# Kernel tuning notes

Hardware: AMD Instinct MI355X
Metric: run time of the kernel (lower is better)

## Reference

```python
import jax, jax.numpy as jnp
import numpy as np

EPS = 1e-5  # BatchNorm eps (eval mode)
K_MAIN = 10
K_CORR = 8
LRELU = 0.2


def _knn_idx(x, k):
    # x: [B, c, n] -> [B, n, k] indices of k nearest neighbors (negative sq. distance top-k)
    inner = -2.0 * jnp.einsum('bcn,bcm->bnm', x, x)
    xx = jnp.sum(x * x, axis=1)                      # [B, n]
    pd = -xx[:, :, None] - inner - xx[:, None, :]    # [B, n, n]
    return jax.lax.top_k(pd, k)[1]


def _gather_neighbors(x, idx):
    # x: [B, c, n], idx: [B, n, k] -> [B, n, k, c]
    xt = jnp.transpose(x, (0, 2, 1))
    B = x.shape[0]
    return xt[jnp.arange(B)[:, None, None], idx]


def _graph_feature(x, k):
    # torch get_graph_feature: cat(neighbor - center, center) -> [B, 2c, n, k]
    idx = _knn_idx(x, k)
    neigh = _gather_neighbors(x, idx)                 # [B, n, k, c]
    xt = jnp.transpose(x, (0, 2, 1))                  # [B, n, c]
    center = jnp.broadcast_to(xt[:, :, None, :], neigh.shape)
    feat = jnp.concatenate([neigh - center, center], axis=-1)
    return jnp.transpose(feat, (0, 3, 1, 2))


def _branch(feat, w, g, b, m, v):
    # 1x1 Conv2d (no bias) + BatchNorm2d (eval) + LeakyReLU(0.2)
    y = jnp.einsum('oc,bcnk->bonk', w, feat)
    s = (g / jnp.sqrt(v + EPS))[None, :, None, None]
    y = (y - m[None, :, None, None]) * s + b[None, :, None, None]
    return jnp.where(y > 0, y, LRELU * y)


def _erase(x, masks, soft, w_e, b_e, g_e, be_e, m_e, v_e):
    # erase_feature: masked-softmax attention pooling + 1x1 conv_erase (conv+BN)
    soft = soft - (1.0 - masks) * 1e8
    sm = jax.nn.softmax(soft, axis=1)                 # [B, n]
    inp = x * masks[:, None, :]
    res = jnp.einsum('bcn,bn->bc', x, sm)             # [B, c]
    y = jnp.einsum('oc,bc->bo', w_e, res) + b_e
    y = (y - m_e) * (g_e / jnp.sqrt(v_e + EPS)) + be_e
    return inp + y[:, :, None]


def _corre_binar(x0_, x2, w_reduce):
    # x0_: [B, c] (detached query), x2: [B, c, n]
    B, c, n = x2.shape
    q = jnp.einsum('oc,bc->bo', w_reduce, x0_)        # conv_reduce (1x1, no bias)
    scale = 1.0 / jnp.sqrt(jnp.asarray(c, x2.dtype))
    f = jnp.einsum('bc,bcn->bn', q, x2) * scale       # [B, n]
    idx8 = _knn_idx(x2, K_CORR)                       # [B, n, 8]
    neigh = _gather_neighbors(x2, idx8)               # [B, n, 8, c]
    fk = jnp.einsum('bc,bnkc->bnk', q, neigh) * scale
    fk = f + jnp.sum(fk, axis=-1)                     # [B, n]
    index = jnp.argmax(fk, axis=1)                    # [B]
    ib = jnp.arange(B)
    masks = jnp.zeros((B, n), x2.dtype).at[ib, index].set(1.0)
    index_k = idx8[ib, index]                         # [B, 8] neighbors of argmax point
    masks = masks.at[ib[:, None], index_k].set(1.0)
    return 1.0 - masks, f


def _forward(x, w_reduce, w_erase, b_erase, g_erase, be_erase, m_erase, v_erase,
             w0, g0, b0, m0, v0, w1, g1, b1, m1, v1):
    b, t, c, n = x.shape
    B = b * t
    x1seq = jnp.concatenate([x[:, 1:], x[:, -1:]], axis=1).reshape(B, c, n)
    ones = jnp.ones((B, n), x.dtype)
    x0 = _erase(x.reshape(B, c, n), ones, ones,
                w_erase, b_erase, g_erase, be_erase, m_erase, v_erase)
    y0 = jnp.max(_branch(_graph_feature(x0, K_MAIN), w0, g0, b0, m0, v0), axis=-1)  # [B, O, n]
    x0_vec = jnp.max(y0, axis=-1)                                                    # [B, O]
    p0 = jnp.concatenate([jnp.max(y0, axis=-1), jnp.mean(y0, axis=-1)], axis=1)
    masks, soft = _corre_binar(jax.lax.stop_gradient(x0_vec), x1seq, w_reduce)
    x1e = _erase(x1seq, masks, soft,
                 w_erase, b_erase, g_erase, be_erase, m_erase, v_erase)
    y1 = jnp.max(_branch(_graph_feature(x1e, K_MAIN), w1, g1, b1, m1, v1), axis=-1)
    p1 = jnp.concatenate([jnp.max(y1, axis=-1), jnp.mean(y1, axis=-1)], axis=1)
    return p0 + p1                                                                   # [B, 2*O]


def setup_inputs() -> dict:
    key = jax.random.key(0)
    ks = jax.random.split(key, 20)
    b, t, c, n, out = 8, 12, 64, 512, 64
    sc = np.sqrt(2.0 / c).astype(np.float32)
    scb = np.sqrt(2.0 / out).astype(np.float32)
    f32 = jnp.float32
    inp = {
        'x': jax.random.normal(ks[0], (b, t, c, n), f32),
        'w_reduce': jax.random.normal(ks[1], (c, c), f32) * sc,
        'w_erase': jax.random.normal(ks[2], (c, c), f32) * sc,
        'b_erase': jax.random.normal(ks[3], (c,), f32) * 0.01,
        'g_erase': jax.random.uniform(ks[4], (c,), f32, 0.5, 1.5),
        'be_erase': jax.random.normal(ks[5], (c,), f32) * 0.1,
        'm_erase': jax.random.normal(ks[6], (c,), f32) * 0.1,
        'v_erase': jax.random.uniform(ks[7], (c,), f32, 0.5, 1.5),
        'w0': jax.random.normal(ks[8], (out, 2 * c), f32) * scb,
        'g0': jax.random.uniform(ks[9], (out,), f32, 0.5, 1.5),
        'b0': jax.random.normal(ks[10], (out,), f32) * 0.1,
        'm0': jax.random.normal(ks[11], (out,), f32) * 0.1,
        'v0': jax.random.uniform(ks[12], (out,), f32, 0.5, 1.5),
        'w1': jax.random.normal(ks[13], (out, 2 * c), f32) * scb,
        'g1': jax.random.uniform(ks[14], (out,), f32, 0.5, 1.5),
        'b1': jax.random.normal(ks[15], (out,), f32) * 0.1,
        'm1': jax.random.normal(ks[16], (out,), f32) * 0.1,
        'v1': jax.random.uniform(ks[17], (out,), f32, 0.5, 1.5),
    }
    return inp


def reference(x, w_reduce, w_erase, b_erase, g_erase, be_erase, m_erase, v_erase,
              w0, g0, b0, m0, v0, w1, g1, b1, m1, v1):
    return _forward(x, w_reduce, w_erase, b_erase, g_erase, be_erase, m_erase, v_erase,
                    w0, g0, b0, m0, v0, w1, g1, b1, m1, v1)
```

## Files before the change

### kernel.cpp

```cpp
#include <hip/hip_runtime.h>
#include <math.h>

#define EPS 1e-5f

typedef _Float16 half8 __attribute__((ext_vector_type(8)));
typedef float f32x4 __attribute__((ext_vector_type(4)));


__device__ __forceinline__ int src_row(int bq) {
    int b = bq / 12, t = bq - b * 12;
    int t2 = (t + 1 < 12) ? (t + 1) : 11;
    return b * 12 + t2;
}

__global__ __launch_bounds__(256) void prep_kernel(
    const float* __restrict__ X,
    _Float16* __restrict__ H, _Float16* __restrict__ L, float* __restrict__ xn,
    const float* __restrict__ w0, const float* __restrict__ w1,
    _Float16* __restrict__ wh0, _Float16* __restrict__ wl0,
    _Float16* __restrict__ wh1, _Float16* __restrict__ wl1,
    const float* __restrict__ w_e, const float* __restrict__ b_e,
    const float* __restrict__ g_e, const float* __restrict__ be_e,
    const float* __restrict__ m_e, const float* __restrict__ v_e,
    float* __restrict__ bias0)
{
    __shared__ float lds[64 * 65];
    __shared__ float xnp[4 * 64];
    __shared__ float part[256];
    __shared__ float res[64];
    __shared__ float sy[64];
    int raw = blockIdx.x;
    int tid = threadIdx.x;
    if (raw >= 768) {
        int bq = raw - 768;
        int c = tid >> 2, p = tid & 3;
        const float* xb = X + (size_t)bq * 32768 + c * 512 + p * 128;
        float acc = 0.f;
        for (int ii = 0; ii < 128; ii += 4) {
            float4 v = *(const float4*)(xb + ii);
            acc += v.x + v.y + v.z + v.w;
        }
        part[tid] = acc;
        __syncthreads();
        if (p == 0) res[c] = (part[tid] + part[tid+1] + part[tid+2] + part[tid+3]) * (1.f/512.f);
        __syncthreads();
        if (tid < 64) {
            float a = b_e[tid];
            for (int cc = 0; cc < 64; ++cc) a += w_e[tid*64+cc] * res[cc];
            float s = g_e[tid] / sqrtf(v_e[tid] + EPS);
            sy[tid] = (a - m_e[tid]) * s + be_e[tid];
        }
        __syncthreads();
        if (tid < 64) {
            float a = 0.f;
            for (int cc = 0; cc < 64; ++cc) a += w0[tid * 128 + 64 + cc] * sy[cc];
            bias0[bq * 64 + tid] = a;
        }
        return;
    }
    int bq = raw % 96;
    int ct = raw / 96;
    const float* Xb = X + (size_t)bq * 32768 + ct * 64;
    for (int p = 0; p < 16; ++p) {
        int t = p * 256 + tid;
        int c = t >> 6, col = t & 63;
        lds[c * 65 + col] = Xb[c * 512 + col];
    }
    __syncthreads();
    int col = tid & 63, g = tid >> 6;
    half8 hv[2], lv[2];
    float s = 0.f;
    #pragma unroll
    for (int k = 0; k < 16; ++k) {
        int c = g * 16 + k;
        float v = lds[c * 65 + col];
        _Float16 h = (_Float16)v;
        _Float16 lo = (_Float16)(v - (float)h);
        hv[k >> 3][k & 7] = h;
        lv[k >> 3][k & 7] = lo;
        s += v * v;
    }
    size_t obase = (size_t)bq * 32768 + ((size_t)(ct * 8 + 2 * g) * 64 + col) * 8;
    *(half8*)(H + obase) = hv[0];
    *(half8*)(H + obase + 512) = hv[1];
    *(half8*)(L + obase) = lv[0];
    *(half8*)(L + obase + 512) = lv[1];
    xnp[g * 64 + col] = s;
    __syncthreads();
    if (tid < 64)
        xn[bq * 512 + ct * 64 + tid] =
            xnp[tid] + xnp[64 + tid] + xnp[128 + tid] + xnp[192 + tid];
    if (raw < 2) {
        const float* W = raw ? w1 : w0;
        _Float16* WH = raw ? wh1 : wh0;
        _Float16* WL = raw ? wl1 : wl0;
        for (int t = tid; t < 8192; t += 256) {
            int o = t >> 6, c = t & 63;
            float v = (o < 64) ? W[o * 128 + c]
                               : (W[(o - 64) * 128 + 64 + c] - W[(o - 64) * 128 + c]);
            _Float16 h = (_Float16)v;
            WH[t] = h;
            WL[t] = (_Float16)(v - (float)h);
        }
    }
}

__global__ __launch_bounds__(256, 4) void knn_kernel(
    const _Float16* __restrict__ H, const _Float16* __restrict__ L,
    const float* __restrict__ xn,
    unsigned short* __restrict__ idx_out, unsigned short* __restrict__ key_out)
{
    __shared__ float4 jbuf[2048];
    __shared__ float sxn[512];
    int raw = blockIdx.x;
    int bq = raw % 96;
    int itile = raw / 96;
    int tid = threadIdx.x, w = tid >> 6, l = tid & 63;
    int lane16 = l & 15, quad = l >> 4;
    const size_t base = (size_t)bq * 32768;
    const _Float16* Hb = H + base;
    const _Float16* Lb = L + base;

    int irow = itile * 64 + w * 16 + lane16;
    size_t bo = ((size_t)(itile * 8 + quad) * 64 + (w * 16 + lane16)) * 8;
    half8 Bh0 = *(const half8*)(Hb + bo);
    half8 Bh1 = *(const half8*)(Hb + bo + 2048);
    half8 Bl0 = *(const half8*)(Lb + bo);
    half8 Bl1 = *(const half8*)(Lb + bo + 2048);

    unsigned kv[20];
    #pragma unroll
    for (int qq = 0; qq < 20; ++qq) kv[qq] = 0u;

    auto casu = [](unsigned& a, unsigned& b) {
        unsigned mn = __builtin_elementwise_min(a, b);
        unsigned mx = __builtin_elementwise_max(a, b);
        a = mn; b = mx;
    };

    const float* xnb = xn + bq * 512;
    float4* jbH = jbuf;
    float4* jbL = jbuf + 1024;
    {
        const float4* gh = (const float4*)(Hb);
        const float4* gl = (const float4*)(Lb);
        jbH[tid] = gh[tid]; jbH[256 + tid] = gh[256 + tid];
        jbL[tid] = gl[tid]; jbL[256 + tid] = gl[256 + tid];
        sxn[tid] = xnb[tid]; sxn[256 + tid] = xnb[256 + tid];
    }
    __syncthreads();
    for (int jt = 0; jt < 8; ++jt) {
        int cur = jt & 1;
        float4 pa0, pa1, pb0, pb1;
        if (jt < 7) {
            const float4* gh = (const float4*)(Hb + (jt + 1) * 4096);
            const float4* gl = (const float4*)(Lb + (jt + 1) * 4096);
            pa0 = gh[tid]; pa1 = gh[256 + tid];
            pb0 = gl[tid]; pb1 = gl[256 + tid];
        }
        const _Float16* jH = (const _Float16*)(jbH + cur * 512);
        const _Float16* jL = (const _Float16*)(jbL + cur * 512);
        unsigned scb = (unsigned)((7 - jt) << 4);
        unsigned d[16];
        #pragma unroll
        for (int g = 0; g < 4; ++g) {
            int u = quad * 64 + g * 16 + lane16;
            half8 Ah0 = *(const half8*)(jH + (size_t)u * 8);
            half8 Ah1 = *(const half8*)(jH + (size_t)u * 8 + 2048);
            half8 Al0 = *(const half8*)(jL + (size_t)u * 8);
            half8 Al1 = *(const half8*)(jL + (size_t)u * 8 + 2048);
            f32x4 acc = {0.f, 0.f, 0.f, 0.f};
            acc = __builtin_amdgcn_mfma_f32_16x16x32_f16(Ah0, Bh0, acc, 0, 0, 0);
            acc = __builtin_amdgcn_mfma_f32_16x16x32_f16(Ah1, Bh1, acc, 0, 0, 0);
            acc = __builtin_amdgcn_mfma_f32_16x16x32_f16(Al0, Bh0, acc, 0, 0, 0);
            acc = __builtin_amdgcn_mfma_f32_16x16x32_f16(Al1, Bh1, acc, 0, 0, 0);
            acc = __builtin_amdgcn_mfma_f32_16x16x32_f16(Ah0, Bl0, acc, 0, 0, 0);
            acc = __builtin_amdgcn_mfma_f32_16x16x32_f16(Ah1, Bl1, acc, 0, 0, 0);
            int jb = jt * 64 + g * 16 + quad * 4;
            float4 xn4 = *(const float4*)&sxn[jb];
            #pragma unroll
            for (int r = 0; r < 4; ++r) {
                float xnr = (r == 0 ? xn4.x : r == 1 ? xn4.y : r == 2 ? xn4.z : xn4.w);
                float sc = fmaf(2.f, acc[r], -xnr);
                int bi = __float_as_int(sc);
                unsigned u2 = (unsigned)(bi ^ ((bi >> 31) | 0x80000000));
                int slot = g * 4 + r;
                d[slot] = (u2 & 0xFFFFFF80u) | (scb | (unsigned)(15 - slot));
            }
        }
        #pragma unroll
        for (int p = 1; p < 16; p <<= 1) {
            #pragma unroll
            for (int k = p; k >= 1; k >>= 1) {
                #pragma unroll
                for (int j = k & (p - 1); j + k < 16; j += 2 * k) {
                    #pragma unroll
                    for (int i = 0; i < k; ++i) {
                        if ((i + j + k < 16) &&
                            ((i + j) / (2 * p) == (i + j + k) / (2 * p)))
                            casu(d[i + j], d[i + j + k]);
                    }
                }
            }
        }
        #pragma unroll
        for (int i = 0; i < 16; ++i)
            kv[i] = __builtin_elementwise_max(kv[i], d[15 - i]);
        casu(kv[0],kv[16]); casu(kv[1],kv[17]); casu(kv[2],kv[18]); casu(kv[3],kv[19]);
        casu(kv[0],kv[8]);  casu(kv[1],kv[9]);  casu(kv[2],kv[10]); casu(kv[3],kv[11]);
        casu(kv[4],kv[12]); casu(kv[5],kv[13]); casu(kv[6],kv[14]); casu(kv[7],kv[15]);
        casu(kv[0],kv[4]);  casu(kv[1],kv[5]);  casu(kv[2],kv[6]);  casu(kv[3],kv[7]);
        casu(kv[8],kv[12]); casu(kv[9],kv[13]); casu(kv[10],kv[14]); casu(kv[11],kv[15]);
        casu(kv[0],kv[2]);  casu(kv[1],kv[3]);  casu(kv[4],kv[6]);  casu(kv[5],kv[7]);
        casu(kv[8],kv[10]); casu(kv[9],kv[11]); casu(kv[12],kv[14]); casu(kv[13],kv[15]);
        casu(kv[16],kv[18]); casu(kv[17],kv[19]);
        casu(kv[0],kv[1]);  casu(kv[2],kv[3]);  casu(kv[4],kv[5]);  casu(kv[6],kv[7]);
        casu(kv[8],kv[9]);  casu(kv[10],kv[11]); casu(kv[12],kv[13]); casu(kv[14],kv[15]);
        casu(kv[16],kv[17]); casu(kv[18],kv[19]);

        if (jt < 7) {
            jbH[(1 - cur) * 512 + tid] = pa0; jbH[(1 - cur) * 512 + 256 + tid] = pa1;
            jbL[(1 - cur) * 512 + tid] = pb0; jbL[(1 - cur) * 512 + 256 + tid] = pb1;
        }
        __syncthreads();
    }
    unsigned* MVb = (unsigned*)jbuf;
    #pragma unroll
    for (int qq = 0; qq < 20; ++qq)
        MVb[w * 1344 + (lane16 * 4 + quad) * 21 + qq] = kv[qq];
    __syncthreads();
    if (quad == 0) {
        const unsigned* MV = (const unsigned*)jbuf + w * 1344 + lane16 * 84;
        int p0 = 19, p1 = 19, p2 = 19, p3 = 19;
        unsigned v0 = MV[19], v1 = MV[21 + 19], v2 = MV[42 + 19], v3 = MV[63 + 19];
        unsigned short* op = idx_out + ((size_t)bq * 512 + irow) * 20;
        unsigned short* kp = key_out + ((size_t)bq * 512 + irow) * 20;
        for (int t = 0; t < 20; ++t) {
            int bc = 0; unsigned bv = v0;
            if (v1 > bv) { bv = v1; bc = 1; }
            if (v2 > bv) { bv = v2; bc = 2; }
            if (v3 > bv) { bv = v3; bc = 3; }
            int bits = (int)(bv & 127u), jtv = 7 - (bits >> 4), cod = 15 - (bits & 15);
            int j = jtv * 64 + ((cod >> 2) << 4) + bc * 4 + (cod & 3);
            op[t] = (unsigned short)j;
            kp[t] = (unsigned short)(bv >> 16);
            if (bc == 0)      { --p0; v0 = MV[p0 < 0 ? 0 : p0]; }
            else if (bc == 1) { --p1; v1 = MV[21 + (p1 < 0 ? 0 : p1)]; }
            else if (bc == 2) { --p2; v2 = MV[42 + (p2 < 0 ? 0 : p2)]; }
            else              { --p3; v3 = MV[63 + (p3 < 0 ? 0 : p3)]; }
        }
    }
}

__global__ __launch_bounds__(1024) void derive_kernel(
    const float* __restrict__ x, const float* __restrict__ x0vec,
    const float* __restrict__ w_reduce,
    const unsigned short* __restrict__ idxA, const unsigned short* __restrict__ keyA,
    const float* __restrict__ xn,
    const float* __restrict__ w_e, const float* __restrict__ b_e,
    const float* __restrict__ g_e, const float* __restrict__ be_e,
    const float* __restrict__ m_e, const float* __restrict__ v_e,
    const float* __restrict__ w1,
    unsigned short* __restrict__ idxB, float* __restrict__ masks_out,
    float* __restrict__ bias1_out)
{
    __shared__ unsigned short sja[512 * 20];
    __shared__ unsigned short ska[512 * 20];
    __shared__ float ss[512];
    __shared__ float sw8[512];
    __shared__ float smask[512];
    __shared__ float xnl[512];
    __shared__ float pl[1024];
    __shared__ float sxv[64], sq[64], sres[64], syy[64];
    __shared__ float redv[8];
    __shared__ int   redi[8];
    __shared__ float redf[8];
    __shared__ float redf2[8];
    __shared__ int mlist[12];
    __shared__ int nmin[12];
    __shared__ int s_mcnt, s_need;

    int bq = blockIdx.x;
    int row = src_row(bq);
    int tid = threadIdx.x;
    int w = tid >> 6, l = tid & 63;
    const float* Xb = x + (size_t)row * 32768;

    {
        const unsigned* gja = (const unsigned*)(idxA + (size_t)row * 10240);
        const unsigned* gka = (const unsigned*)(keyA + (size_t)row * 10240);
        unsigned* dja = (unsigned*)sja;
        unsigned* dka = (unsigned*)ska;
        #pragma unroll
        for (int t = 0; t < 5; ++t) dja[t * 1024 + tid] = gja[t * 1024 + tid];
        #pragma unroll
        for (int t = 0; t < 5; ++t) dka[t * 1024 + tid] = gka[t * 1024 + tid];
    }
    if (tid < 512) { xnl[tid] = xn[row * 512 + tid]; smask[tid] = 1.0f; }
    if (tid < 64) sxv[tid] = x0vec[bq * 64 + tid];
    __syncthreads();
    {
        int o = tid >> 4, c0 = (tid & 15) * 4;
        const float* wr = w_reduce + o * 64 + c0;
        pl[tid] = wr[0]*sxv[c0] + wr[1]*sxv[c0+1] + wr[2]*sxv[c0+2] + wr[3]*sxv[c0+3];
    }
    __syncthreads();
    if (tid < 64) {
        float a = 0.f;
        #pragma unroll
        for (int s = 0; s < 16; ++s) a += pl[tid * 16 + s];
        sq[tid] = a;
    }
    __syncthreads();
    {
        int i = tid >> 1, h = tid & 1;
        float a = 0.f;
        #pragma unroll
        for (int k = 0; k < 32; ++k) {
            int c = h * 32 + k;
            a += sq[c] * Xb[c * 512 + i];
        }
        a += __shfl_xor(a, 1);
        if (h == 0) ss[i] = a * 0.125f;
    }
    __syncthreads();
    if (tid < 512) {
        float a = ss[tid];
        const unsigned short* ip = &sja[tid * 20];
        #pragma unroll
        for (int q = 0; q < 8; ++q) a += ss[ip[q]];
        sw8[tid] = a;
    }
    __syncthreads();
    {
        float bv = -3.4e38f; int bi = 0x7fffffff;
        if (tid < 512) { bv = sw8[tid]; bi = tid; }
        #pragma unroll
        for (int off = 32; off >= 1; off >>= 1) {
            float ov = __shfl_down(bv, off);
            int oi = __shfl_down(bi, off);
            if (ov > bv || (ov == bv && oi < bi)) { bv = ov; bi = oi; }
        }
        if (l == 0 && w < 8) { redv[w] = bv; redi[w] = bi; }
    }
    __syncthreads();
    if (tid == 0) {
        float Bv = redv[0]; int Bi = redi[0];
        for (int ww = 1; ww < 8; ++ww)
            if (redv[ww] > Bv || (redv[ww] == Bv && redi[ww] < Bi)) { Bv = redv[ww]; Bi = redi[ww]; }
        smask[Bi] = 0.f;
        const unsigned short* ip = &sja[Bi * 20];
        int c[9];
        c[0] = Bi;
        for (int q = 0; q < 8; ++q) { int j = ip[q]; smask[j] = 0.f; c[q + 1] = j; }
        for (int i2 = 1; i2 < 9; ++i2) {
            int v = c[i2]; int j2 = i2 - 1;
            while (j2 >= 0 && c[j2] > v) { c[j2 + 1] = c[j2]; --j2; }
            c[j2 + 1] = v;
        }
        int mc = 0, prev = -1;
        for (int i2 = 0; i2 < 9; ++i2)
            if (c[i2] != prev) { mlist[mc++] = c[i2]; prev = c[i2]; }
        s_mcnt = mc;
        s_need = 10 - mc;
    }
    __syncthreads();
    int mcreg = s_mcnt, need = s_need;
    float sval = -3.4e38f;
    if (tid < 512) {
        masks_out[bq * 512 + tid] = smask[tid];
        sval = ss[tid] - (1.f - smask[tid]) * 1e8f;
    }
    {
        float m = sval;
        #pragma unroll
        for (int off = 32; off >= 1; off >>= 1) m = fmaxf(m, __shfl_down(m, off));
        if (l == 0 && w < 8) redf[w] = m;
    }
    __syncthreads();
    float mx = fmaxf(fmaxf(fmaxf(redf[0], redf[1]), fmaxf(redf[2], redf[3])),
                     fmaxf(fmaxf(redf[4], redf[5]), fmaxf(redf[6], redf[7])));
// ... 34 lines not shown
    }
    __syncthreads();
    {
        int o = tid >> 4, c0 = (tid & 15) * 4;
        const float* wr = w_e + o * 64 + c0;
        pl[tid] = wr[0]*sres[c0] + wr[1]*sres[c0+1] + wr[2]*sres[c0+2] + wr[3]*sres[c0+3];
    }
    __syncthreads();
    if (tid < 64) {
        float a = b_e[tid];
        #pragma unroll
        for (int s = 0; s < 16; ++s) a += pl[tid * 16 + s];
        float sc2 = g_e[tid] / sqrtf(v_e[tid] + EPS);
        syy[tid] = (a - m_e[tid]) * sc2 + be_e[tid];
    }
    __syncthreads();
    {
        int o = tid >> 4, c0 = (tid & 15) * 4;
        const float* wr = w1 + o * 128 + 64 + c0;
        pl[tid] = wr[0]*syy[c0] + wr[1]*syy[c0+1] + wr[2]*syy[c0+2] + wr[3]*syy[c0+3];
    }
    __syncthreads();
    if (tid < 64) {
        float a = 0.f;
        #pragma unroll
        for (int s = 0; s < 16; ++s) a += pl[tid * 16 + s];
        bias1_out[bq * 64 + tid] = a;
    }
    if (w == 0) {
        float v[8]; int id[8];
        #pragma unroll
        for (int k = 0; k < 8; ++k) {
            int j = l * 8 + k;
            v[k] = (smask[j] != 0.f) ? xnl[j] : 3.4e38f;
            id[k] = j;
        }
        for (int r = 0; r < need; ++r) {
            float bv = v[0]; int bi = id[0];
            #pragma unroll
            for (int k = 1; k < 8; ++k)
                if (v[k] < bv || (v[k] == bv && id[k] < bi)) { bv = v[k]; bi = id[k]; }
            #pragma unroll
            for (int off = 32; off >= 1; off >>= 1) {
                float ov = __shfl_xor(bv, off);
                int oi = __shfl_xor(bi, off);
                if (ov < bv || (ov == bv && oi < bi)) { bv = ov; bi = oi; }
            }
            if (l == 0) nmin[r] = bi;
            #pragma unroll
            for (int k = 0; k < 8; ++k)
                if (id[k] == bi) v[k] = 3.4e38f;
        }
    }
    __syncthreads();
    if (tid < 512) {
        int i = tid;
        unsigned short tmp[10];
        if (smask[i] == 0.f) {
            int t2 = 0;
            for (int k2 = 0; k2 < mcreg; ++k2) tmp[t2++] = (unsigned short)mlist[k2];
            for (int r = 0; t2 < 10; ++r) tmp[t2++] = (unsigned short)nmin[r];
        } else {
            const unsigned short* ja = &sja[i * 20];
            const unsigned short* ka = &ska[i * 20];
            int pa = 0, pb = 0;
            for (int t2 = 0; t2 < 10; ++t2) {
                while (smask[ja[pa]] == 0.f) ++pa;
                unsigned kva = ka[pa];
                int jva = ja[pa];
                bool takeA = (pb >= mcreg) || (kva > 0x8000u) ||
                             (kva == 0x8000u && jva < mlist[pb]);
                if (takeA) { tmp[t2] = (unsigned short)jva; ++pa; }
                else       { tmp[t2] = (unsigned short)mlist[pb]; ++pb; }
            }
        }
        unsigned* op = (unsigned*)(idxB + (size_t)bq * 5120 + (size_t)i * 10);
        #pragma unroll
        for (int k2 = 0; k2 < 5; ++k2)
            op[k2] = (unsigned)tmp[2 * k2] | ((unsigned)tmp[2 * k2 + 1] << 16);
    }
}

template<int ACC>
__global__ void __attribute__((amdgpu_flat_work_group_size(256, 256), amdgpu_waves_per_eu(2, 4)))
fused_branch_kernel(
    const _Float16* __restrict__ H, const _Float16* __restrict__ L,
    const _Float16* __restrict__ WH, const _Float16* __restrict__ WL,
    const unsigned short* __restrict__ idx, int istride,
    const float* __restrict__ masks, int remap,
    const float* __restrict__ bias,
    const float* __restrict__ g, const float* __restrict__ bb,
    const float* __restrict__ mm, const float* __restrict__ vv,
    float* __restrict__ out_p, float* __restrict__ vec_out)
{
    __shared__ float ldsA[8 * 512];
    __shared__ float ldsB[8 * 512];
    __shared__ unsigned short ldsIdx[512 * 10];
    __shared__ float smask[512];
    int bq = blockIdx.x, ob = blockIdx.y * 8;
    int row = remap ? src_row(bq) : bq;
    bool use_mask = (masks != nullptr);
    int tid = threadIdx.x, w = tid >> 6, l = tid & 63;
    int lane16 = l & 15, quad = l >> 4;
    const size_t base = (size_t)row * 32768;
    unsigned idreg[10];
    if (istride == 10) {
        const unsigned* gp = (const unsigned*)idx + (size_t)bq * 2560;
        #pragma unroll
        for (int k = 0; k < 10; ++k) idreg[k] = gp[tid + k * 256];
    } else {
        const unsigned* gp = (const unsigned*)idx + (size_t)bq * 5120;
        #pragma unroll
        for (int k = 0; k < 10; ++k) {
            int d = tid + k * 256;
            int i = d / 5, r = d - i * 5;
            idreg[k] = gp[i * 10 + r];
        }
    }
    if (use_mask) {
        smask[tid] = masks[bq * 512 + tid];
        smask[tid + 256] = masks[bq * 512 + tid + 256];
        __syncthreads();
    }
    {
        int wrow = (lane16 < 8) ? (ob + lane16) : (64 + ob + (lane16 - 8));
        size_t woff = (size_t)wrow * 64 + quad * 8;
        half8 Ah0 = *(const half8*)(WH + woff);
        half8 Ah1 = *(const half8*)(WH + woff + 32);
        half8 Al0 = *(const half8*)(WL + woff);
        half8 Al1 = *(const half8*)(WL + woff + 32);
        float* dst = (quad < 2) ? ldsA : ldsB;
        int pb = (quad & 1) * 2;
        for (int k = 0; k < 8; ++k) {
            int it = w * 8 + k;
            size_t off = base + (((size_t)(it >> 2) * 8 + quad) * 64 + (it & 3) * 16 + lane16) * 8;
            half8 Xh0 = *(const half8*)(H + off);
            half8 Xh1 = *(const half8*)(H + off + 2048);
            half8 Xl0 = *(const half8*)(L + off);
            half8 Xl1 = *(const half8*)(L + off + 2048);
            if (use_mask) {
                float m = smask[it * 16 + lane16];
                if (m == 0.f) {
                    half8 z = {};
                    Xh0 = z; Xh1 = z; Xl0 = z; Xl1 = z;
                }
            }
            f32x4 acc = {0.f, 0.f, 0.f, 0.f};
            acc = __builtin_amdgcn_mfma_f32_16x16x32_f16(Ah0, Xh0, acc, 0, 0, 0);
            acc = __builtin_amdgcn_mfma_f32_16x16x32_f16(Ah1, Xh1, acc, 0, 0, 0);
            acc = __builtin_amdgcn_mfma_f32_16x16x32_f16(Ah0, Xl0, acc, 0, 0, 0);
            acc = __builtin_amdgcn_mfma_f32_16x16x32_f16(Ah1, Xl1, acc, 0, 0, 0);
            acc = __builtin_amdgcn_mfma_f32_16x16x32_f16(Al0, Xh0, acc, 0, 0, 0);
            acc = __builtin_amdgcn_mfma_f32_16x16x32_f16(Al1, Xh1, acc, 0, 0, 0);
            int j = it * 16 + lane16;
            #pragma unroll
            for (int r = 0; r < 4; ++r)
                dst[((pb + (r >> 1)) * 512 + j) * 2 + (r & 1)] = acc[r];
        }
    }
    {
        unsigned* dp = (unsigned*)ldsIdx;
        #pragma unroll
        for (int k = 0; k < 10; ++k) dp[tid + k * 256] = idreg[k];
    }
    __syncthreads();
    float ssr[2], str[2];
    #pragma unroll
    for (int oo = 0; oo < 2; ++oo) {
        int o = ob + w * 2 + oo;
        float sc = g[o] / sqrtf(vv[o] + EPS);
        ssr[oo] = sc;
        str[oo] = bb[o] - mm[o] * sc + bias[bq * 64 + o] * sc;
    }
    float omax[2], osum[2];
    #pragma unroll
    for (int oo = 0; oo < 2; ++oo) { omax[oo] = -3.4e38f; osum[oo] = 0.f; }
    const float2* A2 = ((const float2*)ldsA) + w * 512;
    const float2* B2 = ((const float2*)ldsB) + w * 512;
    for (int s = 0; s < 8; ++s) {
        int i = l + 64 * s;
        const unsigned* ip32 = (const unsigned*)ldsIdx + i * 5;
        unsigned pr0 = ip32[0], pr1 = ip32[1], pr2 = ip32[2], pr3 = ip32[3], pr4 = ip32[4];
        int idr[10];
        idr[0] = pr0 & 0xffff; idr[1] = pr0 >> 16;
        idr[2] = pr1 & 0xffff; idr[3] = pr1 >> 16;
        idr[4] = pr2 & 0xffff; idr[5] = pr2 >> 16;
        idr[6] = pr3 & 0xffff; idr[7] = pr3 >> 16;
        idr[8] = pr4 & 0xffff; idr[9] = pr4 >> 16;
        float2 v0 = A2[idr[0]];
        float mx0 = v0.x, mx1 = v0.y;
        #pragma unroll
        for (int q = 1; q < 10; ++q) {
            float2 vq = A2[idr[q]];
            mx0 = fmaxf(mx0, vq.x);
            mx1 = fmaxf(mx1, vq.y);
        }
        float2 bv = B2[i];
        float val0 = (mx0 + bv.x) * ssr[0] + str[0];
        float val1 = (mx1 + bv.y) * ssr[1] + str[1];
        float y0 = val0 > 0.f ? val0 : 0.2f * val0;
        float y1 = val1 > 0.f ? val1 : 0.2f * val1;
        omax[0] = fmaxf(omax[0], y0); osum[0] += y0;
        omax[1] = fmaxf(omax[1], y1); osum[1] += y1;
    }
    #pragma unroll
    for (int oo = 0; oo < 2; ++oo) {
        float M = omax[oo], S = osum[oo];
        #pragma unroll
        for (int off = 32; off >= 1; off >>= 1) {
            M = fmaxf(M, __shfl_down(M, off));
            S += __shfl_down(S, off);
        }
        if (l == 0) {
            int o = ob + w * 2 + oo;
            float* po = out_p + bq * 128;
            if (ACC) {
                po[o] += M;
                po[64 + o] += S * (1.f / 512.f);
            } else {
                po[o] = M;
                po[64 + o] = S * (1.f / 512.f);
                vec_out[bq * 64 + o] = M;
            }
        }
    }
}

extern "C" void kernel_launch(void* const* d_in, const int* in_sizes, int n_in,
                              void* d_out, int out_size, void* d_ws, size_t ws_size,
                              hipStream_t stream)
{
    const float* x        = (const float*)d_in[0];
    const float* w_reduce = (const float*)d_in[1];
    const float* w_erase  = (const float*)d_in[2];
    const float* b_erase  = (const float*)d_in[3];
    const float* g_erase  = (const float*)d_in[4];
    const float* be_erase = (const float*)d_in[5];
    const float* m_erase  = (const float*)d_in[6];
    const float* v_erase  = (const float*)d_in[7];
    const float* w0 = (const float*)d_in[8];
    const float* g0 = (const float*)d_in[9];
    const float* b0 = (const float*)d_in[10];
    const float* m0 = (const float*)d_in[11];
    const float* v0 = (const float*)d_in[12];
    const float* w1 = (const float*)d_in[13];
    const float* g1 = (const float*)d_in[14];
    const float* b1 = (const float*)d_in[15];
    const float* m1 = (const float*)d_in[16];
    const float* v1 = (const float*)d_in[17];
    float* out = (float*)d_out;
    char* ws = (char*)d_ws;

    _Float16* h0 = (_Float16*)(ws);
    _Float16* l0 = (_Float16*)(ws + 6291456);
    unsigned short* idxA = (unsigned short*)(ws + 12582912);
    unsigned short* keyA = (unsigned short*)(ws + 14548992);
    unsigned short* idxB = (unsigned short*)(ws + 16515072);
    float* xn0   = (float*)(ws + 17498112);
    float* bias0 = (float*)(ws + 17694720);
    float* bias1 = (float*)(ws + 17719296);
    float* x0vec = (float*)(ws + 17743872);
    float* masks = (float*)(ws + 17768448);
    _Float16* wh0 = (_Float16*)(ws + 17965056);
    _Float16* wl0 = (_Float16*)(ws + 17981440);
    _Float16* wh1 = (_Float16*)(ws + 17997824);
    _Float16* wl1 = (_Float16*)(ws + 18014208);

    (void)in_sizes; (void)n_in; (void)out_size; (void)ws_size;

    prep_kernel<<<864, 256, 0, stream>>>(x, h0, l0, xn0, w0, w1, wh0, wl0, wh1, wl1,
                                         w_erase, b_erase, g_erase, be_erase, m_erase, v_erase, bias0);
    knn_kernel<<<768, 256, 0, stream>>>(h0, l0, xn0, idxA, keyA);
    fused_branch_kernel<0><<<dim3(96, 8), 256, 0, stream>>>(h0, l0, wh0, wl0, idxA, 20,
                                                            nullptr, 0, bias0,
                                                            g0, b0, m0, v0, out, x0vec);
    derive_kernel<<<96, 1024, 0, stream>>>(x, x0vec, w_reduce, idxA, keyA, xn0,
                                           w_erase, b_erase, g_erase, be_erase, m_erase, v_erase,
                                           w1, idxB, masks, bias1);
    fused_branch_kernel<1><<<dim3(96, 8), 256, 0, stream>>>(h0, l0, wh1, wl1, idxB, 10,
                                                            masks, 1, bias1,
                                                            g1, b1, m1, v1, out, nullptr);
}
```

Measured before the change: 182.3 us.

## Precompute both branch conv projections inside kNN kernel and stream them to gather kernels

The per-point 1x1-conv projections for both edge-conv branches are now computed once per point inside the kNN kernel, reusing its already-loaded fp16 hi/lo registers, and written to four fp32 workspace buffers. The branch kernels no longer recompute the MFMA projections. They load the precomputed tiles from global memory, multiplying by the mask in the masked case. This removes duplicated MFMA work, since each branch kernel previously recomputed the projections for every output block. The cost is about 50 MB of extra workspace traffic, and the kNN kernel's occupancy hint drops from 4 to 3 blocks per EU.

Result: slower. 202.5 us (+11.1%).

```diff
diff --git a/kernel.cpp b/kernel.cpp
--- a/kernel.cpp
+++ b/kernel.cpp
@@ -105,10 +105,14 @@
     }
 }
 
-__global__ __launch_bounds__(256, 4) void knn_kernel(
+__global__ __launch_bounds__(256, 3) void knn_kernel(
     const _Float16* __restrict__ H, const _Float16* __restrict__ L,
     const float* __restrict__ xn,
-    unsigned short* __restrict__ idx_out, unsigned short* __restrict__ key_out)
+    unsigned short* __restrict__ idx_out, unsigned short* __restrict__ key_out,
+    const _Float16* __restrict__ wh0, const _Float16* __restrict__ wl0,
+    const _Float16* __restrict__ wh1, const _Float16* __restrict__ wl1,
+    float* __restrict__ c0A, float* __restrict__ c0B,
+    float* __restrict__ c1A, float* __restrict__ c1B)
 {
     __shared__ float4 jbuf[2048];
     __shared__ float sxn[512];
@@ -128,10 +132,6 @@
     half8 Bl0 = *(const half8*)(Lb + bo);
     half8 Bl1 = *(const half8*)(Lb + bo + 2048);
 
-    unsigned kv[20];
-    #pragma unroll
-    for (int qq = 0; qq < 20; ++qq) kv[qq] = 0u;
-
     auto casu = [](unsigned& a, unsigned& b) {
         unsigned mn = __builtin_elementwise_min(a, b);
         unsigned mx = __builtin_elementwise_max(a, b);
@@ -148,6 +148,41 @@
         jbL[tid] = gl[tid]; jbL[256 + tid] = gl[256 + tid];
         sxn[tid] = xnb[tid]; sxn[256 + tid] = xnb[256 + tid];
     }
+    {
+        int pb = (quad & 1) * 2;
+        #pragma unroll
+        for (int cv = 0; cv < 2; ++cv) {
+            const _Float16* WH = cv ? wh1 : wh0;
+            const _Float16* WL = cv ? wl1 : wl0;
+            float* dAp = (cv ? c1A : c0A) + (size_t)bq * 32768;
+            float* dBp = (cv ? c1B : c0B) + (size_t)bq * 32768;
+            float* dst = (quad < 2) ? dAp : dBp;
+            #pragma unroll
+            for (int ob8 = 0; ob8 < 8; ++ob8) {
+                int ob = ob8 * 8;
+                int wrow = (lane16 < 8) ? (ob + lane16) : (64 + ob + (lane16 - 8));
+                size_t woff = (size_t)wrow * 64 + quad * 8;
+                half8 Ah0 = *(const half8*)(WH + woff);
+                half8 Ah1 = *(const half8*)(WH + woff + 32);
+                half8 Al0 = *(const half8*)(WL + woff);
+                half8 Al1 = *(const half8*)(WL + woff + 32);
+                f32x4 acc = {0.f, 0.f, 0.f, 0.f};
+                acc = __builtin_amdgcn_mfma_f32_16x16x32_f16(Ah0, Bh0, acc, 0, 0, 0);
+                acc = __builtin_amdgcn_mfma_f32_16x16x32_f16(Ah1, Bh1, acc, 0, 0, 0);
+                acc = __builtin_amdgcn_mfma_f32_16x16x32_f16(Ah0, Bl0, acc, 0, 0, 0);
+                acc = __builtin_amdgcn_mfma_f32_16x16x32_f16(Ah1, Bl1, acc, 0, 0, 0);
+                acc = __builtin_amdgcn_mfma_f32_16x16x32_f16(Al0, Bh0, acc, 0, 0, 0);
+                acc = __builtin_amdgcn_mfma_f32_16x16x32_f16(Al1, Bh1, acc, 0, 0, 0);
+                float2 v01 = {acc[0], acc[1]};
+                float2 v23 = {acc[2], acc[3]};
+                *(float2*)(dst + ((size_t)((ob8 * 4 + pb) * 512 + irow) * 2)) = v01;
+                *(float2*)(dst + ((size_t)((ob8 * 4 + pb + 1) * 512 + irow) * 2)) = v23;
+            }
+        }
+    }
+    unsigned kv[20];
+    #pragma unroll
+    for (int qq = 0; qq < 20; ++qq) kv[qq] = 0u;
     __syncthreads();
     for (int jt = 0; jt < 8; ++jt) {
         int cur = jt & 1;
@@ -497,10 +532,8 @@
 }
 
 template<int ACC>
-__global__ void __attribute__((amdgpu_flat_work_group_size(256, 256), amdgpu_waves_per_eu(2, 4)))
-fused_branch_kernel(
-    const _Float16* __restrict__ H, const _Float16* __restrict__ L,
-    const _Float16* __restrict__ WH, const _Float16* __restrict__ WL,
+__global__ __launch_bounds__(256) void gather_branch_kernel(
+    const float* __restrict__ cA, const float* __restrict__ cB,
     const unsigned short* __restrict__ idx, int istride,
     const float* __restrict__ masks, int remap,
     const float* __restrict__ bias,
@@ -512,12 +545,10 @@
     __shared__ float ldsB[8 * 512];
     __shared__ unsigned short ldsIdx[512 * 10];
     __shared__ float smask[512];
-    int bq = blockIdx.x, ob = blockIdx.y * 8;
+    int bq = blockIdx.x, ob8 = blockIdx.y;
     int row = remap ? src_row(bq) : bq;
     bool use_mask = (masks != nullptr);
     int tid = threadIdx.x, w = tid >> 6, l = tid & 63;
-    int lane16 = l & 15, quad = l >> 4;
-    const size_t base = (size_t)row * 32768;
     unsigned idreg[10];
     if (istride == 10) {
         const unsigned* gp = (const unsigned*)idx + (size_t)bq * 2560;
@@ -532,45 +563,28 @@
             idreg[k] = gp[i * 10 + r];
         }
     }
+    const float* gA = cA + (size_t)row * 32768 + (size_t)ob8 * 4096;
+    const float* gB = cB + (size_t)row * 32768 + (size_t)ob8 * 4096;
     if (use_mask) {
         smask[tid] = masks[bq * 512 + tid];
         smask[tid + 256] = masks[bq * 512 + tid + 256];
         __syncthreads();
-    }
-    {
-        int wrow = (lane16 < 8) ? (ob + lane16) : (64 + ob + (lane16 - 8));
-        size_t woff = (size_t)wrow * 64 + quad * 8;
-        half8 Ah0 = *(const half8*)(WH + woff);
-        half8 Ah1 = *(const half8*)(WH + woff + 32);
-        half8 Al0 = *(const half8*)(WL + woff);
-        half8 Al1 = *(const half8*)(WL + woff + 32);
-        float* dst = (quad < 2) ? ldsA : ldsB;
-        int pb = (quad & 1) * 2;
-        for (int k = 0; k < 8; ++k) {
-            int it = w * 8 + k;
-            size_t off = base + (((size_t)(it >> 2) * 8 + quad) * 64 + (it & 3) * 16 + lane16) * 8;
-            half8 Xh0 = *(const half8*)(H + off);
-            half8 Xh1 = *(const half8*)(H + off + 2048);
-            half8 Xl0 = *(const half8*)(L + off);
-            half8 Xl1 = *(const half8*)(L + off + 2048);
-            if (use_mask) {
-                float m = smask[it * 16 + lane16];
-                if (m == 0.f) {
-                    half8 z = {};
-                    Xh0 = z; Xh1 = z; Xl0 = z; Xl1 = z;
-                }
-            }
-            f32x4 acc = {0.f, 0.f, 0.f, 0.f};
-            acc = __builtin_amdgcn_mfma_f32_16x16x32_f16(Ah0, Xh0, acc, 0, 0, 0);
-            acc = __builtin_amdgcn_mfma_f32_16x16x32_f16(Ah1, Xh1, acc, 0, 0, 0);
-            acc = __builtin_amdgcn_mfma_f32_16x16x32_f16(Ah0, Xl0, acc, 0, 0, 0);
-            acc = __builtin_amdgcn_mfma_f32_16x16x32_f16(Ah1, Xl1, acc, 0, 0, 0);
-            acc = __builtin_amdgcn_mfma_f32_16x16x32_f16(Al0, Xh0, acc, 0, 0, 0);
-            acc = __builtin_amdgcn_mfma_f32_16x16x32_f16(Al1, Xh1, acc, 0, 0, 0);
-            int j = it * 16 + lane16;
-            #pragma unroll
-            for (int r = 0; r < 4; ++r)
-                dst[((pb + (r >> 1)) * 512 + j) * 2 + (r & 1)] = acc[r];
+        #pragma unroll
+        for (int k = 0; k < 16; ++k) {
+            int t = tid + k * 256;
+            float m = smask[(t >> 1) & 511];
+            ldsA[t] = gA[t] * m;
+            ldsB[t] = gB[t] * m;
+        }
+    } else {
+        float4* dA4 = (float4*)ldsA;
+        float4* dB4 = (float4*)ldsB;
+        const float4* gA4 = (const float4*)gA;
+        const float4* gB4 = (const float4*)gB;
+        #pragma unroll
+        for (int k = 0; k < 4; ++k) {
+            dA4[tid + k * 256] = gA4[tid + k * 256];
+            dB4[tid + k * 256] = gB4[tid + k * 256];
         }
     }
     {
@@ -579,6 +593,7 @@
         for (int k = 0; k < 10; ++k) dp[tid + k * 256] = idreg[k];
     }
     __syncthreads();
+    int ob = ob8 * 8;
     float ssr[2], str[2];
     #pragma unroll
     for (int oo = 0; oo < 2; ++oo) {
@@ -680,19 +695,24 @@
     _Float16* wl0 = (_Float16*)(ws + 17981440);
     _Float16* wh1 = (_Float16*)(ws + 17997824);
     _Float16* wl1 = (_Float16*)(ws + 18014208);
+    float* c0A = (float*)(ws + 18030592);
+    float* c0B = (float*)(ws + 30613504);
+    float* c1A = (float*)(ws + 43196416);
+    float* c1B = (float*)(ws + 55779328);
 
     (void)in_sizes; (void)n_in; (void)out_size; (void)ws_size;
 
     prep_kernel<<<864, 256, 0, stream>>>(x, h0, l0, xn0, w0, w1, wh0, wl0, wh1, wl1,
                                          w_erase, b_erase, g_erase, be_erase, m_erase, v_erase, bias0);
-    knn_kernel<<<768, 256, 0, stream>>>(h0, l0, xn0, idxA, keyA);
-    fused_branch_kernel<0><<<dim3(96, 8), 256, 0, stream>>>(h0, l0, wh0, wl0, idxA, 20,
-                                                            nullptr, 0, bias0,
-                                                            g0, b0, m0, v0, out, x0vec);
+    knn_kernel<<<768, 256, 0, stream>>>(h0, l0, xn0, idxA, keyA,
+                                        wh0, wl0, wh1, wl1, c0A, c0B, c1A, c1B);
+    gather_branch_kernel<0><<<dim3(96, 8), 256, 0, stream>>>(c0A, c0B, idxA, 20,
+                                                             nullptr, 0, bias0,
+                                                             g0, b0, m0, v0, out, x0vec);
     derive_kernel<<<96, 1024, 0, stream>>>(x, x0vec, w_reduce, idxA, keyA, xn0,
                                            w_erase, b_erase, g_erase, be_erase, m_erase, v_erase,
                                            w1, idxB, masks, bias1);
-    fused_branch_kernel<1><<<dim3(96, 8), 256, 0, stream>>>(h0, l0, wh1, wl1, idxB, 10,
-                                                            masks, 1, bias1,
-                                                            g1, b1, m1, v1, out, nullptr);
+    gather_branch_kernel<1><<<dim3(96, 8), 256, 0, stream>>>(c1A, c1B, idxB, 10,
+                                                             masks, 1, bias1,
+                                                             g1, b1, m1, v1, out, nullptr);
 }
```

## Split KNN candidate range across two blocks and merge partial top-k downstream

Applied to the files above, without the earlier changes.

The KNN kernel now splits each row's 512 candidates into two halves handled by separate blocks, doubling the grid, halving LDS, and raising occupancy to 5 blocks per CU. The four per-quad sorted lists are merged with register shuffles and bitonic cleanup instead of an LDS-based serial merge, and each half writes 20 packed keys with the index embedded. Consumers (the fused branch kernel and derive kernel) merge the two partial top-20 lists themselves. This removes the serial scalar merge and LDS staging, but adds merge work and more global traffic in the consumers.

Result: slower. 189.1 us (+3.7%).

```diff
diff --git a/kernel.cpp b/kernel.cpp
--- a/kernel.cpp
+++ b/kernel.cpp
@@ -11,6 +11,25 @@
     int b = bq / 12, t = bq - b * 12;
     int t2 = (t + 1 < 12) ? (t + 1) : 11;
     return b * 12 + t2;
+}
+
+__device__ __forceinline__ void cleanup20(unsigned (&kv)[20]) {
+    auto casu = [](unsigned& a, unsigned& b) {
+        unsigned mn = __builtin_elementwise_min(a, b);
+        unsigned mx = __builtin_elementwise_max(a, b);
+        a = mn; b = mx;
+    };
+    casu(kv[0],kv[16]); casu(kv[1],kv[17]); casu(kv[2],kv[18]); casu(kv[3],kv[19]);
+    casu(kv[0],kv[8]);  casu(kv[1],kv[9]);  casu(kv[2],kv[10]); casu(kv[3],kv[11]);
+    casu(kv[4],kv[12]); casu(kv[5],kv[13]); casu(kv[6],kv[14]); casu(kv[7],kv[15]);
+    casu(kv[0],kv[4]);  casu(kv[1],kv[5]);  casu(kv[2],kv[6]);  casu(kv[3],kv[7]);
+    casu(kv[8],kv[12]); casu(kv[9],kv[13]); casu(kv[10],kv[14]); casu(kv[11],kv[15]);
+    casu(kv[0],kv[2]);  casu(kv[1],kv[3]);  casu(kv[4],kv[6]);  casu(kv[5],kv[7]);
+    casu(kv[8],kv[10]); casu(kv[9],kv[11]); casu(kv[12],kv[14]); casu(kv[13],kv[15]);
+    casu(kv[16],kv[18]); casu(kv[17],kv[19]);
+    casu(kv[0],kv[1]);  casu(kv[2],kv[3]);  casu(kv[4],kv[5]);  casu(kv[6],kv[7]);
+    casu(kv[8],kv[9]);  casu(kv[10],kv[11]); casu(kv[12],kv[13]); casu(kv[14],kv[15]);
+    casu(kv[16],kv[17]); casu(kv[18],kv[19]);
 }
 
 __global__ __launch_bounds__(256) void prep_kernel(
@@ -105,16 +124,18 @@
     }
 }
 
-__global__ __launch_bounds__(256, 4) void knn_kernel(
+__global__ __launch_bounds__(256, 5) void knn_kernel(
     const _Float16* __restrict__ H, const _Float16* __restrict__ L,
     const float* __restrict__ xn,
-    unsigned short* __restrict__ idx_out, unsigned short* __restrict__ key_out)
+    unsigned* __restrict__ key_out)
 {
-    __shared__ float4 jbuf[2048];
-    __shared__ float sxn[512];
+    __shared__ float4 jbuf[1024];
+    __shared__ float sxn[256];
     int raw = blockIdx.x;
-    int bq = raw % 96;
-    int itile = raw / 96;
+    int bq = raw >> 4;
+    int sub = raw & 15;
+    int itile = sub >> 1;
+    int half = sub & 1;
     int tid = threadIdx.x, w = tid >> 6, l = tid & 63;
     int lane16 = l & 15, quad = l >> 4;
     const size_t base = (size_t)bq * 32768;
@@ -128,39 +149,36 @@
     half8 Bl0 = *(const half8*)(Lb + bo);
     half8 Bl1 = *(const half8*)(Lb + bo + 2048);
 
-    unsigned kv[20];
-    #pragma unroll
-    for (int qq = 0; qq < 20; ++qq) kv[qq] = 0u;
-
     auto casu = [](unsigned& a, unsigned& b) {
         unsigned mn = __builtin_elementwise_min(a, b);
         unsigned mx = __builtin_elementwise_max(a, b);
         a = mn; b = mx;
     };
 
-    const float* xnb = xn + bq * 512;
-    float4* jbH = jbuf;
-    float4* jbL = jbuf + 1024;
-    {
-        const float4* gh = (const float4*)(Hb);
-        const float4* gl = (const float4*)(Lb);
-        jbH[tid] = gh[tid]; jbH[256 + tid] = gh[256 + tid];
-        jbL[tid] = gl[tid]; jbL[256 + tid] = gl[256 + tid];
-        sxn[tid] = xnb[tid]; sxn[256 + tid] = xnb[256 + tid];
-    }
-    __syncthreads();
-    for (int jt = 0; jt < 8; ++jt) {
-        int cur = jt & 1;
+    unsigned kv[20];
+    #pragma unroll
+    for (int qq = 0; qq < 20; ++qq) kv[qq] = 0u;
+
+    int jt0 = half * 4;
+    {
+        const float4* gh = (const float4*)(Hb + jt0 * 4096);
+        const float4* gl = (const float4*)(Lb + jt0 * 4096);
+        jbuf[tid] = gh[tid]; jbuf[256 + tid] = gh[256 + tid];
+        jbuf[512 + tid] = gl[tid]; jbuf[768 + tid] = gl[256 + tid];
+        sxn[tid] = xn[bq * 512 + half * 256 + tid];
+    }
+    __syncthreads();
+    for (int t = 0; t < 4; ++t) {
+        int jt = jt0 + t;
         float4 pa0, pa1, pb0, pb1;
-        if (jt < 7) {
+        if (t < 3) {
             const float4* gh = (const float4*)(Hb + (jt + 1) * 4096);
             const float4* gl = (const float4*)(Lb + (jt + 1) * 4096);
             pa0 = gh[tid]; pa1 = gh[256 + tid];
             pb0 = gl[tid]; pb1 = gl[256 + tid];
         }
-        const _Float16* jH = (const _Float16*)(jbH + cur * 512);
-        const _Float16* jL = (const _Float16*)(jbL + cur * 512);
-        unsigned scb = (unsigned)((7 - jt) << 4);
+        const _Float16* jH = (const _Float16*)jbuf;
+        const _Float16* jL = (const _Float16*)(jbuf + 512);
         unsigned d[16];
         #pragma unroll
         for (int g = 0; g < 4; ++g) {
@@ -176,7 +194,7 @@
             acc = __builtin_amdgcn_mfma_f32_16x16x32_f16(Al1, Bh1, acc, 0, 0, 0);
             acc = __builtin_amdgcn_mfma_f32_16x16x32_f16(Ah0, Bl0, acc, 0, 0, 0);
             acc = __builtin_amdgcn_mfma_f32_16x16x32_f16(Ah1, Bl1, acc, 0, 0, 0);
-            int jb = jt * 64 + g * 16 + quad * 4;
+            int jb = t * 64 + g * 16 + quad * 4;
             float4 xn4 = *(const float4*)&sxn[jb];
             #pragma unroll
             for (int r = 0; r < 4; ++r) {
@@ -184,8 +202,7 @@
                 float sc = fmaf(2.f, acc[r], -xnr);
                 int bi = __float_as_int(sc);
                 unsigned u2 = (unsigned)(bi ^ ((bi >> 31) | 0x80000000));
-                int slot = g * 4 + r;
-                d[slot] = (u2 & 0xFFFFFF80u) | (scb | (unsigned)(15 - slot));
+                d[g * 4 + r] = (u2 & 0xFFFFFF00u) | (unsigned)(255 - (jb + r));
             }
         }
         #pragma unroll
@@ -206,56 +223,44 @@
         #pragma unroll
         for (int i = 0; i < 16; ++i)
             kv[i] = __builtin_elementwise_max(kv[i], d[15 - i]);
-        casu(kv[0],kv[16]); casu(kv[1],kv[17]); casu(kv[2],kv[18]); casu(kv[3],kv[19]);
-        casu(kv[0],kv[8]);  casu(kv[1],kv[9]);  casu(kv[2],kv[10]); casu(kv[3],kv[11]);
-        casu(kv[4],kv[12]); casu(kv[5],kv[13]); casu(kv[6],kv[14]); casu(kv[7],kv[15]);
-        casu(kv[0],kv[4]);  casu(kv[1],kv[5]);  casu(kv[2],kv[6]);  casu(kv[3],kv[7]);
-        casu(kv[8],kv[12]); casu(kv[9],kv[13]); casu(kv[10],kv[14]); casu(kv[11],kv[15]);
-        casu(kv[0],kv[2]);  casu(kv[1],kv[3]);  casu(kv[4],kv[6]);  casu(kv[5],kv[7]);
-        casu(kv[8],kv[10]); casu(kv[9],kv[11]); casu(kv[12],kv[14]); casu(kv[13],kv[15]);
-        casu(kv[16],kv[18]); casu(kv[17],kv[19]);
-        casu(kv[0],kv[1]);  casu(kv[2],kv[3]);  casu(kv[4],kv[5]);  casu(kv[6],kv[7]);
-        casu(kv[8],kv[9]);  casu(kv[10],kv[11]); casu(kv[12],kv[13]); casu(kv[14],kv[15]);
-        casu(kv[16],kv[17]); casu(kv[18],kv[19]);
-
-        if (jt < 7) {
-            jbH[(1 - cur) * 512 + tid] = pa0; jbH[(1 - cur) * 512 + 256 + tid] = pa1;
-            jbL[(1 - cur) * 512 + tid] = pb0; jbL[(1 - cur) * 512 + 256 + tid] = pb1;
-        }
-        __syncthreads();
-    }
-    unsigned* MVb = (unsigned*)jbuf;
-    #pragma unroll
-    for (int qq = 0; qq < 20; ++qq)
-        MVb[w * 1344 + (lane16 * 4 + quad) * 21 + qq] = kv[qq];
-    __syncthreads();
+        cleanup20(kv);
+
+        if (t < 3) {
+            __syncthreads();
+            jbuf[tid] = pa0; jbuf[256 + tid] = pa1;
+            jbuf[512 + tid] = pb0; jbuf[768 + tid] = pb1;
+            __syncthreads();
+        }
+    }
+    {
+        unsigned ov[20];
+        #pragma unroll
+        for (int i = 0; i < 20; ++i) ov[i] = __shfl_xor(kv[19 - i], 32);
+        #pragma unroll
+        for (int i = 0; i < 20; ++i) kv[i] = __builtin_elementwise_max(kv[i], ov[i]);
+        cleanup20(kv);
+        #pragma unroll
+        for (int i = 0; i < 20; ++i) ov[i] = __shfl_xor(kv[19 - i], 16);
+        #pragma unroll
+        for (int i = 0; i < 20; ++i) kv[i] = __builtin_elementwise_max(kv[i], ov[i]);
+        cleanup20(kv);
+    }
     if (quad == 0) {
-        const unsigned* MV = (const unsigned*)jbuf + w * 1344 + lane16 * 84;
-        int p0 = 19, p1 = 19, p2 = 19, p3 = 19;
-        unsigned v0 = MV[19], v1 = MV[21 + 19], v2 = MV[42 + 19], v3 = MV[63 + 19];
-        unsigned short* op = idx_out + ((size_t)bq * 512 + irow) * 20;
-        unsigned short* kp = key_out + ((size_t)bq * 512 + irow) * 20;
-        for (int t = 0; t < 20; ++t) {
-            int bc = 0; unsigned bv = v0;
-            if (v1 > bv) { bv = v1; bc = 1; }
-            if (v2 > bv) { bv = v2; bc = 2; }
-            if (v3 > bv) { bv = v3; bc = 3; }
-            int bits = (int)(bv & 127u), jtv = 7 - (bits >> 4), cod = 15 - (bits & 15);
-            int j = jtv * 64 + ((cod >> 2) << 4) + bc * 4 + (cod & 3);
-            op[t] = (unsigned short)j;
-            kp[t] = (unsigned short)(bv >> 16);
-            if (bc == 0)      { --p0; v0 = MV[p0 < 0 ? 0 : p0]; }
-            else if (bc == 1) { --p1; v1 = MV[21 + (p1 < 0 ? 0 : p1)]; }
-            else if (bc == 2) { --p2; v2 = MV[42 + (p2 < 0 ? 0 : p2)]; }
-            else              { --p3; v3 = MV[63 + (p3 < 0 ? 0 : p3)]; }
-        }
+        unsigned* op = key_out + ((size_t)bq * 512 + irow) * 40 + half * 20;
+        uint4 s0; s0.x = kv[19]; s0.y = kv[18]; s0.z = kv[17]; s0.w = kv[16];
+        uint4 s1; s1.x = kv[15]; s1.y = kv[14]; s1.z = kv[13]; s1.w = kv[12];
+        uint4 s2; s2.x = kv[11]; s2.y = kv[10]; s2.z = kv[9];  s2.w = kv[8];
+        uint4 s3; s3.x = kv[7];  s3.y = kv[6];  s3.z = kv[5];  s3.w = kv[4];
+        uint4 s4; s4.x = kv[3];  s4.y = kv[2];  s4.z = kv[1];  s4.w = kv[0];
+        ((uint4*)op)[0] = s0; ((uint4*)op)[1] = s1; ((uint4*)op)[2] = s2;
+        ((uint4*)op)[3] = s3; ((uint4*)op)[4] = s4;
     }
 }
 
 __global__ __launch_bounds__(1024) void derive_kernel(
     const float* __restrict__ x, const float* __restrict__ x0vec,
     const float* __restrict__ w_reduce,
-    const unsigned short* __restrict__ idxA, const unsigned short* __restrict__ keyA,
+    const unsigned* __restrict__ keyA,
     const float* __restrict__ xn,
     const float* __restrict__ w_e, const float* __restrict__ b_e,
     const float* __restrict__ g_e, const float* __restrict__ be_e,
@@ -286,17 +291,35 @@
     int w = tid >> 6, l = tid & 63;
     const float* Xb = x + (size_t)row * 32768;
 
-    {
-        const unsigned* gja = (const unsigned*)(idxA + (size_t)row * 10240);
-        const unsigned* gka = (const unsigned*)(keyA + (size_t)row * 10240);
-        unsigned* dja = (unsigned*)sja;
-        unsigned* dka = (unsigned*)ska;
-        #pragma unroll
-        for (int t = 0; t < 5; ++t) dja[t * 1024 + tid] = gja[t * 1024 + tid];
-        #pragma unroll
-        for (int t = 0; t < 5; ++t) dka[t * 1024 + tid] = gka[t * 1024 + tid];
-    }
-    if (tid < 512) { xnl[tid] = xn[row * 512 + tid]; smask[tid] = 1.0f; }
+    if (tid < 512) {
+        const uint4* r4 = (const uint4*)(keyA + ((size_t)row * 512 + tid) * 40);
+        unsigned fa[20], fb[20];
+        *(uint4*)&fa[0]  = r4[0]; *(uint4*)&fa[4]  = r4[1]; *(uint4*)&fa[8]  = r4[2];
+        *(uint4*)&fa[12] = r4[3]; *(uint4*)&fa[16] = r4[4];
+        *(uint4*)&fb[0]  = r4[5]; *(uint4*)&fb[4]  = r4[6]; *(uint4*)&fb[8]  = r4[7];
+        *(uint4*)&fb[12] = r4[8]; *(uint4*)&fb[16] = r4[9];
+        unsigned A[20], B[20];
+        #pragma unroll
+        for (int i = 0; i < 20; ++i) {
+            unsigned va = fa[19 - i], vb = fb[19 - i];
+            A[i] = (va & 0xFFFFFE00u) | 0x100u | (va & 0xFFu);
+            B[i] = (vb & 0xFFFFFE00u) | (vb & 0xFFu);
+        }
+        #pragma unroll
+        for (int i = 0; i < 20; ++i) A[i] = __builtin_elementwise_max(A[i], B[19 - i]);
+        cleanup20(A);
+        unsigned* pj = (unsigned*)&sja[tid * 20];
+        unsigned* pk = (unsigned*)&ska[tid * 20];
+        #pragma unroll
+        for (int k2 = 0; k2 < 10; ++k2) {
+            unsigned v0 = A[19 - 2 * k2], v1 = A[18 - 2 * k2];
+            unsigned j0 = 511u - (v0 & 511u), j1 = 511u - (v1 & 511u);
+            pj[k2] = j0 | (j1 << 16);
+            pk[k2] = (v0 >> 16) | ((v1 >> 16) << 16);
+        }
+        xnl[tid] = xn[row * 512 + tid];
+        smask[tid] = 1.0f;
+    }
     if (tid < 64) sxv[tid] = x0vec[bq * 64 + tid];
     __syncthreads();
     {
@@ -501,7 +524,8 @@
 fused_branch_kernel(
     const _Float16* __restrict__ H, const _Float16* __restrict__ L,
     const _Float16* __restrict__ WH, const _Float16* __restrict__ WL,
-    const unsigned short* __restrict__ idx, int istride,
+    const unsigned* __restrict__ keyR,
+    const unsigned short* __restrict__ idx10,
     const float* __restrict__ masks, int remap,
     const float* __restrict__ bias,
     const float* __restrict__ g, const float* __restrict__ bb,
@@ -519,18 +543,35 @@
     int lane16 = l & 15, quad = l >> 4;
     const size_t base = (size_t)row * 32768;
     unsigned idreg[10];
-    if (istride == 10) {
-        const unsigned* gp = (const unsigned*)idx + (size_t)bq * 2560;
+    if (keyR) {
+        #pragma unroll
+        for (int qq = 0; qq < 2; ++qq) {
+            int q = tid * 2 + qq;
+            const unsigned* rowp = keyR + ((size_t)bq * 512 + q) * 40;
+            unsigned a[10], b[10];
+            *(uint4*)&a[0] = ((const uint4*)rowp)[0];
+            *(uint4*)&a[4] = ((const uint4*)rowp)[1];
+            a[8] = rowp[8]; a[9] = rowp[9];
+            *(uint4*)&b[0] = ((const uint4*)rowp)[5];
+            *(uint4*)&b[4] = ((const uint4*)rowp)[6];
+            b[8] = rowp[28]; b[9] = rowp[29];
+            unsigned short ids[10];
+            #pragma unroll
+            for (int i = 0; i < 10; ++i) {
+                unsigned va = a[i], vb = b[9 - i];
+                bool tA = va >= vb;
+                unsigned v = tA ? va : vb;
+                ids[i] = (unsigned short)((tA ? 0 : 256) + 255 - (int)(v & 255u));
+            }
+            unsigned* dp = (unsigned*)&ldsIdx[q * 10];
+            #pragma unroll
+            for (int k = 0; k < 5; ++k)
+                dp[k] = (unsigned)ids[2 * k] | ((unsigned)ids[2 * k + 1] << 16);
+        }
+    } else {
+        const unsigned* gp = (const unsigned*)idx10 + (size_t)bq * 2560;
         #pragma unroll
         for (int k = 0; k < 10; ++k) idreg[k] = gp[tid + k * 256];
-    } else {
-        const unsigned* gp = (const unsigned*)idx + (size_t)bq * 5120;
-        #pragma unroll
-        for (int k = 0; k < 10; ++k) {
-            int d = tid + k * 256;
-            int i = d / 5, r = d - i * 5;
-            idreg[k] = gp[i * 10 + r];
-        }
     }
     if (use_mask) {
         smask[tid] = masks[bq * 512 + tid];
@@ -573,7 +614,7 @@
                 dst[((pb + (r >> 1)) * 512 + j) * 2 + (r & 1)] = acc[r];
         }
     }
-    {
+    if (!keyR) {
         unsigned* dp = (unsigned*)ldsIdx;
         #pragma unroll
         for (int k = 0; k < 10; ++k) dp[tid + k * 256] = idreg[k];
@@ -668,31 +709,30 @@
 
     _Float16* h0 = (_Float16*)(ws);
     _Float16* l0 = (_Float16*)(ws + 6291456);
-    unsigned short* idxA = (unsigned short*)(ws + 12582912);
-    unsigned short* keyA = (unsigned short*)(ws + 14548992);
-    unsigned short* idxB = (unsigned short*)(ws + 16515072);
-    float* xn0   = (float*)(ws + 17498112);
-    float* bias0 = (float*)(ws + 17694720);
-    float* bias1 = (float*)(ws + 17719296);
-    float* x0vec = (float*)(ws + 17743872);
-    float* masks = (float*)(ws + 17768448);
-    _Float16* wh0 = (_Float16*)(ws + 17965056);
-    _Float16* wl0 = (_Float16*)(ws + 17981440);
-    _Float16* wh1 = (_Float16*)(ws + 17997824);
-    _Float16* wl1 = (_Float16*)(ws + 18014208);
+    unsigned* keyA = (unsigned*)(ws + 12582912);
+    unsigned short* idxB = (unsigned short*)(ws + 20447232);
+    float* xn0   = (float*)(ws + 21430272);
+    float* bias0 = (float*)(ws + 21626880);
+    float* bias1 = (float*)(ws + 21651456);
+    float* x0vec = (float*)(ws + 21676032);
+    float* masks = (float*)(ws + 21700608);
+    _Float16* wh0 = (_Float16*)(ws + 21897216);
+    _Float16* wl0 = (_Float16*)(ws + 21913600);
+    _Float16* wh1 = (_Float16*)(ws + 21929984);
+    _Float16* wl1 = (_Float16*)(ws + 21946368);
 
     (void)in_sizes; (void)n_in; (void)out_size; (void)ws_size;
 
     prep_kernel<<<864, 256, 0, stream>>>(x, h0, l0, xn0, w0, w1, wh0, wl0, wh1, wl1,
                                          w_erase, b_erase, g_erase, be_erase, m_erase, v_erase, bias0);
-    knn_kernel<<<768, 256, 0, stream>>>(h0, l0, xn0, idxA, keyA);
-    fused_branch_kernel<0><<<dim3(96, 8), 256, 0, stream>>>(h0, l0, wh0, wl0, idxA, 20,
+    knn_kernel<<<1536, 256, 0, stream>>>(h0, l0, xn0, keyA);
+    fused_branch_kernel<0><<<dim3(96, 8), 256, 0, stream>>>(h0, l0, wh0, wl0, keyA, nullptr,
                                                             nullptr, 0, bias0,
                                                             g0, b0, m0, v0, out, x0vec);
-    derive_kernel<<<96, 1024, 0, stream>>>(x, x0vec, w_reduce, idxA, keyA, xn0,
+    derive_kernel<<<96, 1024, 0, stream>>>(x, x0vec, w_reduce, keyA, xn0,
                                            w_erase, b_erase, g_erase, be_erase, m_erase, v_erase,
                                            w1, idxB, masks, bias1);
-    fused_branch_kernel<1><<<dim3(96, 8), 256, 0, stream>>>(h0, l0, wh1, wl1, idxB, 10,
+    fused_branch_kernel<1><<<dim3(96, 8), 256, 0, stream>>>(h0, l0, wh1, wl1, nullptr, idxB,
                                                             masks, 1, bias1,
                                                             g1, b1, m1, v1, out, nullptr);
 }
```
